# Optimization experiments

Measured on AMD Instinct MI355X. Metric: run time of the kernel, lower is better.

Reference implementation:

```python
import jax, jax.numpy as jnp
import numpy as np

B, S, D, H = 4, 2048, 1024, 16
DH = D // H  # 64


def setup_inputs() -> dict:
    key = jax.random.key(0)
    ks = jax.random.split(key, 8)
    scale = 1.0 / np.sqrt(D)  # xavier-ish init for square linears
    return {
        "query": jax.random.normal(ks[0], (B, S, D), jnp.float32),
        "key": jax.random.normal(ks[1], (B, S, D), jnp.float32),
        "value": jax.random.normal(ks[2], (B, S, D), jnp.float32),
        "mask": jax.random.randint(ks[3], (B, 1, 1, S), 0, 2).astype(jnp.bool_),
        "Wq": jax.random.normal(ks[4], (D, D), jnp.float32) * scale,
        "Wk": jax.random.normal(ks[5], (D, D), jnp.float32) * scale,
        "Wv": jax.random.normal(ks[6], (D, D), jnp.float32) * scale,
        "Wo": jax.random.normal(ks[7], (D, D), jnp.float32) * scale,
    }


def _split_heads(x):
    # (B, S, D) -> (B, H, S, DH)
    b, s, _ = x.shape
    return x.reshape(b, s, H, DH).transpose(0, 2, 1, 3)


def reference(query, key, value, mask, Wq, Wk, Wv, Wo):
    # Linear projections (torch Linear: x @ W.T, no bias)
    q = _split_heads(query @ Wq.T)   # (B, H, S, DH)
    k = _split_heads(key @ Wk.T)     # (B, H, S, DH)
    v = _split_heads(value @ Wv.T)   # (B, H, S, DH)

    # Scaled dot-product attention: softmax(QK^T / sqrt(d_head)) V
    scores = jnp.einsum("bhqd,bhkd->bhqk", q, k) / np.sqrt(DH).astype(np.float32)
    # masked_fill_(mask, -1e9): True entries are masked out
    scores = jnp.where(mask, jnp.float32(-1e9), scores)
    attn = jax.nn.softmax(scores, axis=-1)
    # dropout: identity at inference (eval mode)
    ctx = jnp.einsum("bhqk,bhkd->bhqd", attn, v)  # (B, H, S, DH)

    # Merge heads and apply output projection
    ctx = ctx.transpose(0, 2, 1, 3).reshape(query.shape[0], -1, H * DH)
    return ctx @ Wo.T
```

## Files before the change

### kernel.cpp

```cpp
#include <hip/hip_runtime.h>


#define BB 4
#define SS 2048
#define DD 1024
#define HH 16
#define DH 64

typedef __bf16 bf16x8 __attribute__((ext_vector_type(8)));
typedef float floatx4 __attribute__((ext_vector_type(4)));
typedef unsigned short ushortx8 __attribute__((ext_vector_type(8)));
typedef unsigned short ushortx4 __attribute__((ext_vector_type(4)));
typedef unsigned short ushort_t;

__device__ __forceinline__ unsigned short f2bf(float f) {
    unsigned u = __builtin_bit_cast(unsigned, f);
    u += 0x7FFFu + ((u >> 16) & 1u);
    return (unsigned short)(u >> 16);
}

__device__ __forceinline__ bf16x8 ldb(const ushort_t* p) {
    return __builtin_bit_cast(bf16x8, *(const ushortx8*)p);
}

__device__ __forceinline__ void dma16(const ushort_t* g, ushort_t* l) {
    __builtin_amdgcn_global_load_lds(
        (const __attribute__((address_space(1))) unsigned int*)g,
        (__attribute__((address_space(3))) unsigned int*)l, 16, 0, 0);
}

__device__ __forceinline__ floatx4 mfma32(bf16x8 a, bf16x8 b, floatx4 c) {
    return __builtin_amdgcn_mfma_f32_16x16x32_bf16(a, b, c, 0, 0, 0);
}

__device__ __forceinline__ floatx4 fzero() {
    floatx4 z = {0.f, 0.f, 0.f, 0.f};
    return z;
}

__device__ __forceinline__ void cvt_body(const float* __restrict__ in,
                                         ushort_t* __restrict__ out) {
    int i = (blockIdx.x * blockDim.x + threadIdx.x) * 4;
    float4 f = *(const float4*)&in[i];
    ushortx4 o;
    o[0] = f2bf(f.x); o[1] = f2bf(f.y); o[2] = f2bf(f.z); o[3] = f2bf(f.w);
    *(ushortx4*)&out[i] = o;
}

__global__ void cvt3(const float* __restrict__ i0, const float* __restrict__ i1,
                     const float* __restrict__ i2, ushort_t* __restrict__ o0,
                     ushort_t* __restrict__ o1, ushort_t* __restrict__ o2) {
    const float* in = blockIdx.y == 0 ? i0 : blockIdx.y == 1 ? i1 : i2;
    ushort_t* out = blockIdx.y == 0 ? o0 : blockIdx.y == 1 ? o1 : o2;
    cvt_body(in, out);
}

__global__ void cvt4(const float* __restrict__ i0, const float* __restrict__ i1,
                     const float* __restrict__ i2, const float* __restrict__ i3,
                     ushort_t* __restrict__ o0, ushort_t* __restrict__ o1,
                     ushort_t* __restrict__ o2, ushort_t* __restrict__ o3) {
    const float* in = blockIdx.y == 0 ? i0 : blockIdx.y == 1 ? i1
                     : blockIdx.y == 2 ? i2 : i3;
    ushort_t* out = blockIdx.y == 0 ? o0 : blockIdx.y == 1 ? o1
                   : blockIdx.y == 2 ? o2 : o3;
    cvt_body(in, out);
}

__device__ __forceinline__ void gemm_core(
    const ushort_t* __restrict__ Ab, const ushort_t* __restrict__ Bb,
    floatx4 acc[4][4], ushort_t (*As)[128][32], ushort_t (*Bs)[128][32], int tid)
{
    const int wv = tid >> 6, lane = tid & 63;
    const int quad = lane >> 4, lid = lane & 15;
    const int wm = wv & 1, wn = wv >> 1;
    const int r0 = lane >> 2, c0 = (lane & 3) * 8;

#pragma unroll
    for (int i = 0; i < 4; ++i)
#pragma unroll
        for (int j = 0; j < 4; ++j) acc[i][j] = fzero();

#pragma unroll
    for (int s = 0; s < 2; ++s) {
        int seg = wv * 2 + s;
        dma16(&Ab[(size_t)(seg * 16 + r0) * DD + c0], &As[0][seg * 16][0]);
        dma16(&Bb[(size_t)(seg * 16 + r0) * DD + c0], &Bs[0][seg * 16][0]);
    }
    __syncthreads();

    int cur = 0;
    for (int k0 = 0; k0 < DD; k0 += 32) {
        int nxt = cur ^ 1;
        if (k0 + 32 < DD) {
#pragma unroll
            for (int s = 0; s < 2; ++s) {
                int seg = wv * 2 + s;
                dma16(&Ab[(size_t)(seg * 16 + r0) * DD + k0 + 32 + c0], &As[nxt][seg * 16][0]);
                dma16(&Bb[(size_t)(seg * 16 + r0) * DD + k0 + 32 + c0], &Bs[nxt][seg * 16][0]);
            }
        }
        bf16x8 af[4], bfr[4];
#pragma unroll
        for (int mt = 0; mt < 4; ++mt) af[mt] = ldb(&As[cur][wm * 64 + mt * 16 + lid][quad * 8]);
#pragma unroll
        for (int nt = 0; nt < 4; ++nt) bfr[nt] = ldb(&Bs[cur][wn * 64 + nt * 16 + lid][quad * 8]);
#pragma unroll
        for (int mt = 0; mt < 4; ++mt)
#pragma unroll
            for (int nt = 0; nt < 4; ++nt)
                acc[mt][nt] = mfma32(af[mt], bfr[nt], acc[mt][nt]);
        __syncthreads();
        cur = nxt;
    }
}

__global__ __launch_bounds__(256) void gemm_qkv(
    const ushort_t* __restrict__ Qa, const ushort_t* __restrict__ Ka,
    const ushort_t* __restrict__ Va, const ushort_t* __restrict__ Wqkv,
    const int* __restrict__ maskg,
    ushort_t* __restrict__ Qp, ushort_t* __restrict__ Kp, ushort_t* __restrict__ Vtp)
{
    __shared__ ushort_t As[2][128][32];
    __shared__ ushort_t Bs[2][128][32];
    __shared__ ushort_t Ts[4][16][72];

    const int tid = threadIdx.x;
    const int f = blockIdx.x;
    const int logical = (f & 7) * 192 + (f >> 3);
    const int by = logical / 24;
    const int bxx = logical % 24;
    const int which = bxx >> 3;
    const int m0 = by * 128;
    const int n0 = bxx * 128;
    const ushort_t* Ab = (which == 0 ? Qa : which == 1 ? Ka : Va) + (size_t)m0 * DD;
    const ushort_t* Bb = Wqkv + (size_t)n0 * DD;

    floatx4 acc[4][4];
    gemm_core(Ab, Bb, acc, As, Bs, tid);

    const int wv = tid >> 6, lane = tid & 63;
    const int quad = lane >> 4, lid = lane & 15;
    const int wm = wv & 1, wn = wv >> 1;
    const int b = m0 >> 11;
    const int sbase = (m0 & 2047) + wm * 64;
    const int nl0 = n0 - which * 1024 + wn * 64;
    const int sl = lane >> 2, cl = (lane & 3) * 16;

    if (which == 2) {
        const int* maskb = maskg + b * SS;
#pragma unroll
        for (int nt = 0; nt < 4; ++nt) {
#pragma unroll
            for (int mt = 0; mt < 4; ++mt) {
                int sp = sbase + mt * 16 + quad * 4;
                int4 mv = *(const int4*)&maskb[sp];
                ushortx4 o;
                o[0] = mv.x ? (ushort_t)0 : f2bf(acc[mt][nt][0]);
                o[1] = mv.y ? (ushort_t)0 : f2bf(acc[mt][nt][1]);
                o[2] = mv.z ? (ushort_t)0 : f2bf(acc[mt][nt][2]);
                o[3] = mv.w ? (ushort_t)0 : f2bf(acc[mt][nt][3]);
                *(ushortx4*)&Ts[wv][lid][mt * 16 + quad * 4] = o;
            }
            ushortx8 w0 = *(const ushortx8*)&Ts[wv][sl][cl];
            ushortx8 w1 = *(const ushortx8*)&Ts[wv][sl][cl + 8];
            int nl = nl0 + nt * 16 + sl;
            int h = nl >> 6, dh = nl & 63;
            size_t base = (((size_t)b * HH + h) * DH + dh) * SS + sbase + cl;
            *(ushortx8*)&Vtp[base] = w0;
            *(ushortx8*)&Vtp[base + 8] = w1;
        }
    } else {
        ushort_t* P = which ? Kp : Qp;
        const float scl = which ? 1.0f : 0.125f * 1.4426950408889634f;
        const int h = nl0 >> 6;
#pragma unroll
        for (int mt = 0; mt < 4; ++mt) {
#pragma unroll
            for (int nt = 0; nt < 4; ++nt)
#pragma unroll
                for (int r = 0; r < 4; ++r)
                    Ts[wv][quad * 4 + r][nt * 16 + lid] = f2bf(acc[mt][nt][r] * scl);
            ushortx8 w0 = *(const ushortx8*)&Ts[wv][sl][cl];
            ushortx8 w1 = *(const ushortx8*)&Ts[wv][sl][cl + 8];
            int s = sbase + mt * 16 + sl;
            size_t base = (((size_t)b * HH + h) * SS + s) * DH + (nl0 & 63) + cl;
            *(ushortx8*)&P[base] = w0;
            *(ushortx8*)&P[base + 8] = w1;
        }
    }
}

__global__ __launch_bounds__(256) void gemm_o(
    const ushort_t* __restrict__ Cx, const ushort_t* __restrict__ Wo,
    float* __restrict__ Out)
{
    __shared__ ushort_t As[2][128][32];
    __shared__ ushort_t Bs[2][128][32];
    const int tid = threadIdx.x;
    const int f = blockIdx.x;
    const int logical = (f & 7) * 64 + (f >> 3);
    const int by = logical >> 3, bx = logical & 7;
    const int m0 = by * 128;
    const int n0 = bx * 128;

    floatx4 acc[4][4];
    gemm_core(Cx + (size_t)m0 * DD, Wo + (size_t)n0 * DD, acc, As, Bs, tid);

    const int wv = tid >> 6, lane = tid & 63;
    const int quad = lane >> 4, lid = lane & 15;
    const int wm = wv & 1, wn = wv >> 1;
#pragma unroll
    for (int mt = 0; mt < 4; ++mt)
#pragma unroll
        for (int nt = 0; nt < 4; ++nt)
#pragma unroll
            for (int r = 0; r < 4; ++r) {
                int m = m0 + wm * 64 + mt * 16 + quad * 4 + r;
                int n = n0 + wn * 64 + nt * 16 + lid;
                Out[(size_t)m * DD + n] = acc[mt][nt][r];
            }
}

__global__ __launch_bounds__(256) void attn_kernel(
    const ushort_t* __restrict__ Qg, const ushort_t* __restrict__ Kg,
    const ushort_t* __restrict__ Vtg, const int* __restrict__ maskg,
    ushort_t* __restrict__ Ctx)
{
    __shared__ ushort_t Ks[2][64 * 64];
    __shared__ ushort_t Vts[2][64 * 64];
    __shared__ ushort_t fmb[SS];

    const int flat = blockIdx.x;
    const int xcd = flat & 7;
    const int slot = flat >> 3;
    const int bh = xcd * 8 + (slot >> 5);
    const int qc = slot & 31;
    const int b = bh >> 4, h = bh & 15;
    const int tid = threadIdx.x;
    const int wv = tid >> 6, lane = tid & 63;
    const int quad = lane >> 4, lid = lane & 15;

    const ushort_t* Qb = Qg + (size_t)bh * SS * DH;
    const ushort_t* Kb = Kg + (size_t)bh * SS * DH;
    const ushort_t* Vtb = Vtg + (size_t)bh * DH * SS;
    const int* maskb = maskg + b * SS;

    {
        const int k8 = tid * 8;
        int4 ma = *(const int4*)&maskb[k8];
        int4 mb2 = *(const int4*)&maskb[k8 + 4];
        ushortx8 fv;
        fv[0] = ma.x ? (ushort_t)0 : (ushort_t)0x3F80;
        fv[1] = ma.y ? (ushort_t)0 : (ushort_t)0x3F80;
        fv[2] = ma.z ? (ushort_t)0 : (ushort_t)0x3F80;
        fv[3] = ma.w ? (ushort_t)0 : (ushort_t)0x3F80;
        fv[4] = mb2.x ? (ushort_t)0 : (ushort_t)0x3F80;
        fv[5] = mb2.y ? (ushort_t)0 : (ushort_t)0x3F80;
        fv[6] = mb2.z ? (ushort_t)0 : (ushort_t)0x3F80;
        fv[7] = mb2.w ? (ushort_t)0 : (ushort_t)0x3F80;
        *(ushortx8*)&fmb[k8] = fv;
    }

    const int q0 = qc * 64 + wv * 16;

    bf16x8 qf0, qf1;
    {
        const int row = q0 + lid;
        qf0 = ldb(&Qb[(size_t)row * DH + quad * 8]);
        qf1 = ldb(&Qb[(size_t)row * DH + 32 + quad * 8]);
    }

    int offK[2], offV[2];
#pragma unroll
    for (int s = 0; s < 2; ++s) {
        int idx = wv * 128 + s * 64 + lane;
        int row = idx >> 3;
        int c16 = idx & 7;
        int p = (row & 35) | ((row & 12) << 1) | ((row & 16) >> 2);
        int colu = (c16 ^ (row & 7)) << 3;
        offK[s] = p * DH + colu;
        offV[s] = row * SS + colu;
    }

    floatx4 Oacc[4];
    floatx4 Osum = fzero();
#pragma unroll
    for (int i = 0; i < 4; ++i) Oacc[i] = fzero();

    const int swz = (lid & 7) << 3;

    dma16(Kb + offK[0], &Ks[0][(wv * 2 + 0) * 512]);
    dma16(Kb + offK[1], &Ks[0][(wv * 2 + 1) * 512]);
    dma16(Vtb + offV[0], &Vts[0][(wv * 2 + 0) * 512]);
    dma16(Vtb + offV[1], &Vts[0][(wv * 2 + 1) * 512]);
    __syncthreads();

    const ushort_t* Kc = Kb + 64 * DH;
    const ushort_t* Vc = Vtb + 64;
    int cur = 0;

    for (int kc = 0; kc < SS / 64; ++kc) {
        int nxt = cur ^ 1;
        if (kc + 1 < SS / 64) {
            dma16(Kc + offK[0], &Ks[nxt][(wv * 2 + 0) * 512]);
            dma16(Kc + offK[1], &Ks[nxt][(wv * 2 + 1) * 512]);
            dma16(Vc + offV[0], &Vts[nxt][(wv * 2 + 0) * 512]);
            dma16(Vc + offV[1], &Vts[nxt][(wv * 2 + 1) * 512]);
            Kc += 64 * DH;
            Vc += 64;
        }

        floatx4 st[4];
#pragma unroll
        for (int mt = 0; mt < 4; ++mt) {
            const int rb = (mt * 16 + lid) * 64;
            bf16x8 kf0 = ldb(&Ks[cur][rb + ((quad * 8) ^ swz)]);
            bf16x8 kf1 = ldb(&Ks[cur][rb + ((32 + quad * 8) ^ swz)]);
            st[mt] = mfma32(kf1, qf1, mfma32(kf0, qf0, fzero()));
        }

#pragma unroll
        for (int kk = 0; kk < 2; ++kk) {
            bf16x8 pa;
#pragma unroll
            for (int r = 0; r < 4; ++r) {
                pa[r]     = (__bf16)__builtin_amdgcn_exp2f(st[2 * kk][r]);
                pa[r + 4] = (__bf16)__builtin_amdgcn_exp2f(st[2 * kk + 1][r]);
            }
            bf16x8 fm = ldb(&fmb[kc * 64 + kk * 32 + quad * 8]);
            Osum = mfma32(pa, fm, Osum);
#pragma unroll
            for (int nt = 0; nt < 4; ++nt) {
                bf16x8 vb = ldb(&Vts[cur][(nt * 16 + lid) * 64 + ((kk * 32 + quad * 8) ^ swz)]);
                Oacc[nt] = mfma32(pa, vb, Oacc[nt]);
            }
        }
        __syncthreads();
        cur = nxt;
    }

    float inv[4];
#pragma unroll
    for (int r = 0; r < 4; ++r) inv[r] = 1.0f / Osum[r];

#pragma unroll
    for (int nt = 0; nt < 4; ++nt) {
#pragma unroll
        for (int r = 0; r < 4; ++r) {
            int s = q0 + quad * 4 + r;
            int dh = nt * 16 + lid;
            Ctx[(((size_t)b * SS + s) * HH + h) * DH + dh] = f2bf(Oacc[nt][r] * inv[r]);
        }
    }
}

extern "C" void kernel_launch(void* const* d_in, const int* in_sizes, int n_in,
                              void* d_out, int out_size, void* d_ws, size_t ws_size,
                              hipStream_t stream) {
    const float* q  = (const float*)d_in[0];
    const float* k  = (const float*)d_in[1];
    const float* v  = (const float*)d_in[2];
    const int*   mask = (const int*)d_in[3];
    const float* Wq = (const float*)d_in[4];
    const float* Wk = (const float*)d_in[5];
    const float* Wv = (const float*)d_in[6];
    const float* Wo = (const float*)d_in[7];
    float* out = (float*)d_out;

    char* ws = (char*)d_ws;
    const size_t MB = 1024 * 1024;
    ushort_t* Qin  = (ushort_t*)(ws + 0 * MB);
    ushort_t* Kin  = (ushort_t*)(ws + 16 * MB);
    ushort_t* Vin  = (ushort_t*)(ws + 32 * MB);
    ushort_t* Qp   = (ushort_t*)(ws + 48 * MB);
    ushort_t* Kp   = (ushort_t*)(ws + 64 * MB);
    ushort_t* Vtp  = (ushort_t*)(ws + 80 * MB);
    ushort_t* Wqkv = (ushort_t*)(ws + 96 * MB);
    ushort_t* Wob  = (ushort_t*)(ws + 102 * MB);
    ushort_t* Cx   = Qin;

    const int INEL = BB * SS * DD;
    const int WN = DD * DD;
    cvt3<<<dim3(INEL / 1024, 3), 256, 0, stream>>>(q, k, v, Qin, Kin, Vin);
    cvt4<<<dim3(WN / 1024, 4), 256, 0, stream>>>(Wq, Wk, Wv, Wo,
                                                 Wqkv, Wqkv + WN, Wqkv + 2 * WN, Wob);

    gemm_qkv<<<dim3(1536), 256, 0, stream>>>(Qin, Kin, Vin, Wqkv, mask, Qp, Kp, Vtp);
    attn_kernel<<<dim3(2048), 256, 0, stream>>>(Qp, Kp, Vtp, mask, Cx);
    gemm_o<<<dim3(512), 256, 0, stream>>>(Cx, Wob, out);
}
```

Baseline: 344.5 us.

## Process two query tiles per wave in attention to reuse K/V fragments

Each wave now handles 32 query rows (two 16-row groups) instead of 16, so each block covers 128 queries and the grid is halved. K and V fragments read from shared memory and the mask fragment are reused across both groups, halving LDS reads and global K/V loads per query. This raises register use (two sets of accumulators and Q fragments) and halves the block count, which may reduce occupancy or latency hiding.

```diff
diff --git a/kernel.cpp b/kernel.cpp
--- a/kernel.cpp
+++ b/kernel.cpp
@@ -233,8 +233,8 @@
     const int flat = blockIdx.x;
     const int xcd = flat & 7;
     const int slot = flat >> 3;
-    const int bh = xcd * 8 + (slot >> 5);
-    const int qc = slot & 31;
+    const int bh = xcd * 8 + (slot >> 4);
+    const int qc = slot & 15;
     const int b = bh >> 4, h = bh & 15;
     const int tid = threadIdx.x;
     const int wv = tid >> 6, lane = tid & 63;
@@ -261,13 +261,14 @@
         *(ushortx8*)&fmb[k8] = fv;
     }
 
-    const int q0 = qc * 64 + wv * 16;
-
-    bf16x8 qf0, qf1;
-    {
-        const int row = q0 + lid;
-        qf0 = ldb(&Qb[(size_t)row * DH + quad * 8]);
-        qf1 = ldb(&Qb[(size_t)row * DH + 32 + quad * 8]);
+    const int qbase = qc * 128 + wv * 32;
+
+    bf16x8 qf[2][2];
+#pragma unroll
+    for (int g = 0; g < 2; ++g) {
+        const int row = qbase + g * 16 + lid;
+        qf[g][0] = ldb(&Qb[(size_t)row * DH + quad * 8]);
+        qf[g][1] = ldb(&Qb[(size_t)row * DH + 32 + quad * 8]);
     }
 
     int offK[2], offV[2];
@@ -282,10 +283,14 @@
         offV[s] = row * SS + colu;
     }
 
-    floatx4 Oacc[4];
-    floatx4 Osum = fzero();
-#pragma unroll
-    for (int i = 0; i < 4; ++i) Oacc[i] = fzero();
+    floatx4 Oacc[2][4];
+    floatx4 Osum[2];
+#pragma unroll
+    for (int g = 0; g < 2; ++g) {
+        Osum[g] = fzero();
+#pragma unroll
+        for (int i = 0; i < 4; ++i) Oacc[g][i] = fzero();
+    }
 
     const int swz = (lid & 7) << 3;
 
@@ -310,46 +315,53 @@
             Vc += 64;
         }
 
-        floatx4 st[4];
-#pragma unroll
-        for (int mt = 0; mt < 4; ++mt) {
-            const int rb = (mt * 16 + lid) * 64;
-            bf16x8 kf0 = ldb(&Ks[cur][rb + ((quad * 8) ^ swz)]);
-            bf16x8 kf1 = ldb(&Ks[cur][rb + ((32 + quad * 8) ^ swz)]);
-            st[mt] = mfma32(kf1, qf1, mfma32(kf0, qf0, fzero()));
-        }
-
 #pragma unroll
         for (int kk = 0; kk < 2; ++kk) {
-            bf16x8 pa;
+            floatx4 sA[2], sB[2];
+#pragma unroll
+            for (int m2 = 0; m2 < 2; ++m2) {
+                const int mt = kk * 2 + m2;
+                const int rb = (mt * 16 + lid) * 64;
+                bf16x8 kf0 = ldb(&Ks[cur][rb + ((quad * 8) ^ swz)]);
+                bf16x8 kf1 = ldb(&Ks[cur][rb + ((32 + quad * 8) ^ swz)]);
+                sA[m2] = mfma32(kf1, qf[0][1], mfma32(kf0, qf[0][0], fzero()));
+                sB[m2] = mfma32(kf1, qf[1][1], mfma32(kf0, qf[1][0], fzero()));
+            }
+            bf16x8 pa, pb;
 #pragma unroll
             for (int r = 0; r < 4; ++r) {
-                pa[r]     = (__bf16)__builtin_amdgcn_exp2f(st[2 * kk][r]);
-                pa[r + 4] = (__bf16)__builtin_amdgcn_exp2f(st[2 * kk + 1][r]);
+                pa[r]     = (__bf16)__builtin_amdgcn_exp2f(sA[0][r]);
+                pa[r + 4] = (__bf16)__builtin_amdgcn_exp2f(sA[1][r]);
+                pb[r]     = (__bf16)__builtin_amdgcn_exp2f(sB[0][r]);
+                pb[r + 4] = (__bf16)__builtin_amdgcn_exp2f(sB[1][r]);
             }
             bf16x8 fm = ldb(&fmb[kc * 64 + kk * 32 + quad * 8]);
-            Osum = mfma32(pa, fm, Osum);
+            Osum[0] = mfma32(pa, fm, Osum[0]);
+            Osum[1] = mfma32(pb, fm, Osum[1]);
 #pragma unroll
             for (int nt = 0; nt < 4; ++nt) {
                 bf16x8 vb = ldb(&Vts[cur][(nt * 16 + lid) * 64 + ((kk * 32 + quad * 8) ^ swz)]);
-                Oacc[nt] = mfma32(pa, vb, Oacc[nt]);
+                Oacc[0][nt] = mfma32(pa, vb, Oacc[0][nt]);
+                Oacc[1][nt] = mfma32(pb, vb, Oacc[1][nt]);
             }
         }
         __syncthreads();
         cur = nxt;
     }
 
-    float inv[4];
-#pragma unroll
-    for (int r = 0; r < 4; ++r) inv[r] = 1.0f / Osum[r];
-
-#pragma unroll
-    for (int nt = 0; nt < 4; ++nt) {
-#pragma unroll
-        for (int r = 0; r < 4; ++r) {
-            int s = q0 + quad * 4 + r;
-            int dh = nt * 16 + lid;
-            Ctx[(((size_t)b * SS + s) * HH + h) * DH + dh] = f2bf(Oacc[nt][r] * inv[r]);
+#pragma unroll
+    for (int g = 0; g < 2; ++g) {
+        float inv[4];
+#pragma unroll
+        for (int r = 0; r < 4; ++r) inv[r] = 1.0f / Osum[g][r];
+#pragma unroll
+        for (int nt = 0; nt < 4; ++nt) {
+#pragma unroll
+            for (int r = 0; r < 4; ++r) {
+                int s = qbase + g * 16 + quad * 4 + r;
+                int dh = nt * 16 + lid;
+                Ctx[(((size_t)b * SS + s) * HH + h) * DH + dh] = f2bf(Oacc[g][nt][r] * inv[r]);
+            }
         }
     }
 }
@@ -386,6 +398,6 @@
                                                  Wqkv, Wqkv + WN, Wqkv + 2 * WN, Wob);
 
     gemm_qkv<<<dim3(1536), 256, 0, stream>>>(Qin, Kin, Vin, Wqkv, mask, Qp, Kp, Vtp);
-    attn_kernel<<<dim3(2048), 256, 0, stream>>>(Qp, Kp, Vtp, mask, Cx);
+    attn_kernel<<<dim3(1024), 256, 0, stream>>>(Qp, Kp, Vtp, mask, Cx);
     gemm_o<<<dim3(512), 256, 0, stream>>>(Cx, Wob, out);
 }
```

Measured after the change: 340.2 us. No clear change (-1.2%).
